# Performance work log

Hardware: AMD Instinct MI355X
Metric: run time of the kernel (lower is better)

The kernel has to match this reference:

```python
import jax, jax.numpy as jnp
import numpy as np

N, E, G, F_IN, H, C = 50000, 800000, 512, 128, 96, 10
BN_EPS = 1e-5


def _bn(x, w, b):
    # torch BatchNorm1d training-mode forward: batch stats, biased variance
    mu = jnp.mean(x, axis=0)
    var = jnp.var(x, axis=0)
    return (x - mu) * jax.lax.rsqrt(var + BN_EPS) * w + b


def setup_inputs() -> dict:
    key = jax.random.key(0)
    ks = iter(jax.random.split(key, 64))

    def rn(shape, s=0.05):
        return jax.random.normal(next(ks), shape, jnp.float32) * s

    inp = {
        "x": jax.random.normal(next(ks), (N, F_IN), jnp.float32),
        "edge_index": jax.random.randint(next(ks), (2, E), 0, N, dtype=jnp.int32),
        "batch": jnp.sort(jax.random.randint(next(ks), (N,), 0, G, dtype=jnp.int32)),
        "bn_feat_w": jnp.ones((F_IN,), jnp.float32),
        "bn_feat_b": jnp.full((F_IN,), 1e-4, jnp.float32),
        "Wf": rn((F_IN, H)), "bf": jnp.zeros((H,), jnp.float32),
        "bn_fc_w": jnp.ones((H,), jnp.float32),
        "bn_fc_b": jnp.full((H,), 1e-4, jnp.float32),
        "Wl": rn((H, H)), "bl": jnp.zeros((H,), jnp.float32),
        "bn_hid_w": jnp.ones((H,), jnp.float32),
        "bn_hid_b": jnp.full((H,), 1e-4, jnp.float32),
        "Wc": rn((H, C)), "bc": jnp.zeros((C,), jnp.float32),
    }
    for i in range(3):
        inp[f"W1_{i}"] = rn((H, H)); inp[f"b1_{i}"] = jnp.zeros((H,), jnp.float32)
        inp[f"bnw_{i}"] = jnp.ones((H,), jnp.float32)
        inp[f"bnb_{i}"] = jnp.full((H,), 1e-4, jnp.float32)
        inp[f"W2_{i}"] = rn((H, H)); inp[f"b2_{i}"] = jnp.zeros((H,), jnp.float32)
    return inp


def reference(x, edge_index, batch, bn_feat_w, bn_feat_b, Wf, bf,
              W1_0, b1_0, bnw_0, bnb_0, W2_0, b2_0,
              W1_1, b1_1, bnw_1, bnb_1, W2_1, b2_1,
              W1_2, b1_2, bnw_2, bnb_2, W2_2, b2_2,
              bn_fc_w, bn_fc_b, Wl, bl, bn_hid_w, bn_hid_b, Wc, bc):
    src, dst = edge_index[0], edge_index[1]
    h = _bn(x, bn_feat_w, bn_feat_b)
    # GCNConv(gfn=True): pure linear feature transform, no propagation
    h = jax.nn.relu(h @ Wf + bf)
    gin_params = [
        (W1_0, b1_0, bnw_0, bnb_0, W2_0, b2_0),
        (W1_1, b1_1, bnw_1, bnb_1, W2_1, b2_1),
        (W1_2, b1_2, bnw_2, bnb_2, W2_2, b2_2),
    ]
    for W1, b1, bw, bb, W2, b2 in gin_params:
        # GIN: (1+eps)*x + sum-aggregate of neighbor features (eps=0)
        agg = jax.ops.segment_sum(h[src], dst, num_segments=N)  # [N, H]
        m = h + agg
        m = jax.nn.relu(_bn(m @ W1 + b1, bw, bb))
        h = jax.nn.relu(m @ W2 + b2)
    # global_add_pool over graphs
    g = jax.ops.segment_sum(h, batch, num_segments=G)  # [G, H]
    g = jax.nn.relu(_bn(g, bn_fc_w, bn_fc_b) @ Wl + bl)
    g = _bn(g, bn_hid_w, bn_hid_b)
    logits = g @ Wc + bc
    return jax.nn.log_softmax(logits, axis=-1)
```

## Files before the change

### kernel.cpp

```cpp
#include <hip/hip_runtime.h>

#define N_NODES 50000
#define N_EDGES 800000
#define N_GRAPHS 512
#define F_IN 128
#define HDIM 96
#define NCLS 10
#define BN_EPS 1e-5f

#define NPB 128
#define NBUCK2 ((N_NODES + NPB - 1) / NPB)
#define NEB 128
#define EPB ((N_EDGES + NEB - 1) / NEB)

typedef unsigned int u32;
typedef unsigned short u16;
typedef __attribute__((ext_vector_type(8))) short bf16x8;
typedef __attribute__((ext_vector_type(4))) float f32x4;

__device__ __forceinline__ u16 f2bf(float f) {
    u32 u = __float_as_uint(f);
    u32 r = (u + 0x7fffu + ((u >> 16) & 1u)) >> 16;
    return (u16)r;
}
__device__ __forceinline__ float bflo(u32 w) { return __uint_as_float(w << 16); }
__device__ __forceinline__ float bfhi(u32 w) { return __uint_as_float(w & 0xffff0000u); }
__device__ __forceinline__ float bf2f(u16 v) { return __uint_as_float((u32)v << 16); }

template<int NC>
__global__ __launch_bounds__(256) void colstats4_kernel(const float* __restrict__ in,
                                                        float* __restrict__ partials,
                                                        int nrows) {
    constexpr int CG  = NC / 4;
    constexpr int RPB = 256 / CG;
    const int cg = threadIdx.x % CG;
    const int rg = threadIdx.x / CG;
    float4 s = make_float4(0.f, 0.f, 0.f, 0.f);
    float4 q = make_float4(0.f, 0.f, 0.f, 0.f);
    for (int r = blockIdx.x * RPB + rg; r < nrows; r += gridDim.x * RPB) {
        float4 v = *(const float4*)&in[(size_t)r * NC + cg * 4];
        s.x += v.x; s.y += v.y; s.z += v.z; s.w += v.w;
        q.x += v.x * v.x; q.y += v.y * v.y; q.z += v.z * v.z; q.w += v.w * v.w;
    }
    __shared__ float ss[RPB][NC], sq[RPB][NC];
    *(float4*)&ss[rg][cg * 4] = s;
    *(float4*)&sq[rg][cg * 4] = q;
    __syncthreads();
    if (threadIdx.x < NC) {
        float a = 0.f, b = 0.f;
        #pragma unroll
        for (int r = 0; r < RPB; r++) { a += ss[r][threadIdx.x]; b += sq[r][threadIdx.x]; }
        partials[(size_t)blockIdx.x * 2 * NC + threadIdx.x]      = a;
        partials[(size_t)blockIdx.x * 2 * NC + NC + threadIdx.x] = b;
    }
}

template<int NCOLS>
__global__ __launch_bounds__(NCOLS * 8) void reduce_finalize_kernel(
        const float* __restrict__ partials, int nslots,
        const float* __restrict__ w,
        const float* __restrict__ b,
        float* __restrict__ ac, float inv_n) {
    const int k   = threadIdx.x % NCOLS;
    const int grp = threadIdx.x / NCOLS;
    const int stride = 2 * NCOLS;
    float s = 0.f, q = 0.f;
    for (int i = grp; i < nslots; i += 8) {
        s += partials[(size_t)i * stride + k];
        q += partials[(size_t)i * stride + NCOLS + k];
    }
    __shared__ float ss[8][NCOLS], sq[8][NCOLS];
    ss[grp][k] = s; sq[grp][k] = q;
    __syncthreads();
    if (grp == 0) {
        float S = ((ss[0][k] + ss[1][k]) + (ss[2][k] + ss[3][k]))
                + ((ss[4][k] + ss[5][k]) + (ss[6][k] + ss[7][k]));
        float Q = ((sq[0][k] + sq[1][k]) + (sq[2][k] + sq[3][k]))
                + ((sq[4][k] + sq[5][k]) + (sq[6][k] + sq[7][k]));
        float mu  = S * inv_n;
        float var = Q * inv_n - mu * mu;
        float a   = w[k] * rsqrtf(var + BN_EPS);
        ac[k]         = a;
        ac[NCOLS + k] = b[k] - mu * a;
    }
}

#define WPF_BLOCKS 48
#define WPH_BLOCKS 36
__global__ __launch_bounds__(256) void wprep_all_kernel(
        const float* __restrict__ Wf, const float* __restrict__ bf, const float* __restrict__ acX,
        const float* __restrict__ W0a, const float* __restrict__ b0a,
        const float* __restrict__ W0b, const float* __restrict__ b0b,
        const float* __restrict__ W1a, const float* __restrict__ b1a,
        const float* __restrict__ W1b, const float* __restrict__ b1b,
        const float* __restrict__ W2a, const float* __restrict__ b2a,
        const float* __restrict__ W2b, const float* __restrict__ b2b,
        u16* __restrict__ wtF, float* __restrict__ bFm,
        u16* __restrict__ wtbase, float* __restrict__ bmbase) {
    const int tid = threadIdx.x;
    int blk = blockIdx.x;
    if (blk < WPF_BLOCKS) {
        int i = blk * 256 + tid;
        if (i < F_IN * 96) {
            int k = i / 96, n = i % 96;
            wtF[n * F_IN + k] = f2bf(Wf[i] * acX[k]);
        }
        if (blk == 0 && tid < 96) {
            float b = bf[tid];
            for (int k = 0; k < F_IN; k++) b += acX[F_IN + k] * Wf[k * 96 + tid];
            bFm[tid] = b;
        }
        return;
    }
    blk -= WPF_BLOCKS;
    const int s  = blk / WPH_BLOCKS;
    const int b2 = blk % WPH_BLOCKS;
    const float* W; const float* bias;
    switch (s) {
        case 0: W = W0a; bias = b0a; break;
        case 1: W = W0b; bias = b0b; break;
        case 2: W = W1a; bias = b1a; break;
        case 3: W = W1b; bias = b1b; break;
        case 4: W = W2a; bias = b2a; break;
        default: W = W2b; bias = b2b; break;
    }
    u16*   wtb  = wtbase + (size_t)s * 96 * HDIM;
    float* bmod = bmbase + (size_t)s * 96;
    int i = b2 * 256 + tid;
    if (i < HDIM * 96) {
        int k = i / 96, n = i % 96;
        wtb[n * HDIM + k] = f2bf(W[i]);
    }
    if (b2 == 0 && tid < 96) bmod[tid] = bias[tid];
}

__global__ __launch_bounds__(1024) void scan1_fused_kernel(
        const int* __restrict__ inA, int nA, int* __restrict__ tmpA, int* __restrict__ partA,
        const int* __restrict__ inB, int nB, int* __restrict__ tmpB, int* __restrict__ partB,
        int nblkA) {
    const int* in; int n; int* tmp; int* partial; int base;
    if ((int)blockIdx.x < nblkA) { in = inA; n = nA; tmp = tmpA; partial = partA; base = blockIdx.x; }
    else                         { in = inB; n = nB; tmp = tmpB; partial = partB; base = blockIdx.x - nblkA; }
    __shared__ int sh[1024];
    const int i = base * 1024 + threadIdx.x;
    const int d = (i < n) ? in[i] : 0;
    sh[threadIdx.x] = d;
    __syncthreads();
    for (int off = 1; off < 1024; off <<= 1) {
        int v = 0;
        if (threadIdx.x >= off) v = sh[threadIdx.x - off];
        __syncthreads();
        sh[threadIdx.x] += v;
        __syncthreads();
    }
    if (i < n) tmp[i] = sh[threadIdx.x] - d;
    if (threadIdx.x == 1023) partial[base] = sh[1023];
}

__global__ __launch_bounds__(1024) void scan3_fused_kernel(
        const int* __restrict__ tmpA, const int* __restrict__ partA,
        const int* __restrict__ degA, int* __restrict__ row_ptr, int nA, int npA,
        const int* __restrict__ tmpB, const int* __restrict__ partB,
        int* __restrict__ ofs, int nB, int npB, int nblkA) {
    const int* tmp; const int* partial; int n, nparts, base; bool isA;
    if ((int)blockIdx.x < nblkA) { tmp = tmpA; partial = partA; n = nA; nparts = npA; base = blockIdx.x; isA = true; }
    else                         { tmp = tmpB; partial = partB; n = nB; nparts = npB; base = blockIdx.x - nblkA; isA = false; }
    __shared__ int offs;
    if (threadIdx.x < 64) {
        int v = (threadIdx.x < base && (int)threadIdx.x < nparts) ? partial[threadIdx.x] : 0;
        for (int o = 32; o > 0; o >>= 1) v += __shfl_down(v, o, 64);
        if (threadIdx.x == 0) offs = v;
    }
    __syncthreads();
    const int i = base * 1024 + threadIdx.x;
    if (i < n) {
        int v = tmp[i] + offs;
        if (isA) {
            row_ptr[i] = v;
            if (i == n - 1) row_ptr[n] = v + degA[i];
        } else {
            ofs[i] = v;
        }
    }
}

__global__ __launch_bounds__(256) void count_kernel(const int* __restrict__ dst,
                                                    int* __restrict__ deg,
                                                    int* __restrict__ cnt) {
    __shared__ int lc[NBUCK2];
    for (int i = threadIdx.x; i < NBUCK2; i += 256) lc[i] = 0;
    __syncthreads();
    const int lo = blockIdx.x * EPB;
    const int hi = min(lo + EPB, N_EDGES);
    for (int e = lo + threadIdx.x; e < hi; e += 256) {
        int d = dst[e];
        atomicAdd(&lc[d / NPB], 1);
        atomicAdd(&deg[d], 1);
    }
    __syncthreads();
    for (int i = threadIdx.x; i < NBUCK2; i += 256)
        cnt[i * NEB + blockIdx.x] = lc[i];
}

__global__ __launch_bounds__(256) void distribute_kernel(const int* __restrict__ src,
                                                         const int* __restrict__ dst,
                                                         const int* __restrict__ ofs,
                                                         u32* __restrict__ ebuf) {
    __shared__ int lofs[NBUCK2];
    for (int i = threadIdx.x; i < NBUCK2; i += 256) lofs[i] = ofs[i * NEB + blockIdx.x];
    __syncthreads();
    const int lo = blockIdx.x * EPB;
    const int hi = min(lo + EPB, N_EDGES);
    for (int e = lo + threadIdx.x; e < hi; e += 256) {
        int d = dst[e];
        int q = atomicAdd(&lofs[d / NPB], 1);
        ebuf[q] = ((u32)src[e] << 7) | (u32)(d & (NPB - 1));
    }
}

__global__ __launch_bounds__(256) void bucket_fill_kernel(const u32* __restrict__ ebuf,
                                                          const int* __restrict__ ofs,
                                                          const int* __restrict__ row_ptr,
                                                          int* __restrict__ csr) {
    __shared__ int cur[NPB];
    const int p    = blockIdx.x;
    const int base = p * NPB;
    const int nn   = min(NPB, N_NODES - base);
    for (int i = threadIdx.x; i < nn; i += 256) cur[i] = row_ptr[base + i];
    __syncthreads();
    const int e0 = ofs[p * NEB];
    const int e1 = (p + 1 < NBUCK2) ? ofs[(p + 1) * NEB] : N_EDGES;
    for (int e = e0 + threadIdx.x; e < e1; e += 256) {
        u32 v = ebuf[e];
        int pos = atomicAdd(&cur[v & (NPB - 1)], 1);
        csr[pos] = (int)(v >> 7);
    }
}

__global__ __launch_bounds__(256) void aggmm_kernel(const u16* __restrict__ hb,
                                                    const int* __restrict__ row_ptr,
                                                    const int* __restrict__ csr,
                                                    const u16* __restrict__ wt,
                                                    const float* __restrict__ bias,
                                                    float* __restrict__ tf,
                                                    float* __restrict__ partials,
                                                    int nrows) {
    constexpr int KP = HDIM + 8;
    constexpr int KB = HDIM / 32;
    __shared__ u16 wlds[96 * KP];
    __shared__ u16 alds[64 * KP];
    __shared__ float sred[2][4][96];
    const int tid = threadIdx.x;

    for (int i = tid; i < 96 * (HDIM / 8); i += 256) {
        int nn = i / (HDIM / 8), c8 = i % (HDIM / 8);
        *(uint4*)&wlds[nn * KP + c8 * 8] = *(const uint4*)&wt[nn * HDIM + c8 * 8];
    }

    const int w    = tid >> 6;
    const int lane = tid & 63;
    const int r16  = lane & 15;
    const int kg   = lane >> 4;
    const int m0   = w * 16;
    float bn[6];
    #pragma unroll
    for (int nt = 0; nt < 6; nt++) bn[nt] = bias[nt * 16 + r16];
    float scol[6] = {0,0,0,0,0,0}, qcol[6] = {0,0,0,0,0,0};

    const int nchunks = (nrows + 63) / 64;
    for (int chunk = blockIdx.x; chunk < nchunks; chunk += gridDim.x) {
        const int row0 = chunk * 64;
        __syncthreads();
        for (int t = tid; t < 64 * 12; t += 256) {
            const int r  = t / 12, sl = t % 12;
            const int node = row0 + r;
            uint4 ov = make_uint4(0u, 0u, 0u, 0u);
            if (node < nrows) {
                const int p0 = row_ptr[node], p1 = row_ptr[node + 1];
                uint4 sv = *(const uint4*)&hb[(size_t)node * 96 + sl * 8];
                double a0 = bflo(sv.x), a1 = bfhi(sv.x), a2 = bflo(sv.y), a3 = bfhi(sv.y);
                double a4 = bflo(sv.z), a5 = bfhi(sv.z), a6 = bflo(sv.w), a7 = bfhi(sv.w);
                int p = p0;
                for (; p + 4 <= p1; p += 4) {
                    int s0 = csr[p], s1 = csr[p + 1], s2 = csr[p + 2], s3 = csr[p + 3];
                    uint4 v0 = *(const uint4*)&hb[(size_t)s0 * 96 + sl * 8];
                    uint4 v1 = *(const uint4*)&hb[(size_t)s1 * 96 + sl * 8];
                    uint4 v2 = *(const uint4*)&hb[(size_t)s2 * 96 + sl * 8];
                    uint4 v3 = *(const uint4*)&hb[(size_t)s3 * 96 + sl * 8];
                    a0 += bflo(v0.x); a0 += bflo(v1.x); a0 += bflo(v2.x); a0 += bflo(v3.x);
                    a1 += bfhi(v0.x); a1 += bfhi(v1.x); a1 += bfhi(v2.x); a1 += bfhi(v3.x);
                    a2 += bflo(v0.y); a2 += bflo(v1.y); a2 += bflo(v2.y); a2 += bflo(v3.y);
                    a3 += bfhi(v0.y); a3 += bfhi(v1.y); a3 += bfhi(v2.y); a3 += bfhi(v3.y);
                    a4 += bflo(v0.z); a4 += bflo(v1.z); a4 += bflo(v2.z); a4 += bflo(v3.z);
                    a5 += bfhi(v0.z); a5 += bfhi(v1.z); a5 += bfhi(v2.z); a5 += bfhi(v3.z);
                    a6 += bflo(v0.w); a6 += bflo(v1.w); a6 += bflo(v2.w); a6 += bflo(v3.w);
                    a7 += bfhi(v0.w); a7 += bfhi(v1.w); a7 += bfhi(v2.w); a7 += bfhi(v3.w);
                }
                for (; p < p1; p++) {
                    int s = csr[p];
                    uint4 v = *(const uint4*)&hb[(size_t)s * 96 + sl * 8];
                    a0 += bflo(v.x); a1 += bfhi(v.x); a2 += bflo(v.y); a3 += bfhi(v.y);
                    a4 += bflo(v.z); a5 += bfhi(v.z); a6 += bflo(v.w); a7 += bfhi(v.w);
                }
                ov.x = (u32)f2bf((float)a0) | ((u32)f2bf((float)a1) << 16);
                ov.y = (u32)f2bf((float)a2) | ((u32)f2bf((float)a3) << 16);
                ov.z = (u32)f2bf((float)a4) | ((u32)f2bf((float)a5) << 16);
                ov.w = (u32)f2bf((float)a6) | ((u32)f2bf((float)a7) << 16);
            }
            *(uint4*)&alds[r * KP + sl * 8] = ov;
        }
        __syncthreads();

        bf16x8 af[KB];
        #pragma unroll
        for (int kb = 0; kb < KB; kb++)
            af[kb] = *(const bf16x8*)&alds[(m0 + r16) * KP + kb * 32 + kg * 8];

        f32x4 acc[6];
        #pragma unroll
        for (int nt = 0; nt < 6; nt++) acc[nt] = (f32x4){bn[nt], bn[nt], bn[nt], bn[nt]};
        #pragma unroll
        for (int kb = 0; kb < KB; kb++) {
            #pragma unroll
            for (int nt = 0; nt < 6; nt++) {
                bf16x8 bfr = *(const bf16x8*)&wlds[(nt * 16 + r16) * KP + kb * 32 + kg * 8];
                acc[nt] = __builtin_amdgcn_mfma_f32_16x16x32_bf16(af[kb], bfr, acc[nt], 0, 0, 0);
            }
        }

        const int gr0  = row0 + m0 + kg * 4;
        const bool full = (gr0 + 3 < nrows);
        #pragma unroll
        for (int nt = 0; nt < 6; nt++) {
            const int n = nt * 16 + r16;
            #pragma unroll
            for (int rr = 0; rr < 4; rr++) {
                const int gr = gr0 + rr;
                if (full || gr < nrows) {
                    float v = acc[nt][rr];
                    tf[(size_t)gr * 96 + n] = v;
                    scol[nt] += v; qcol[nt] += v * v;
                }
            }
        }
    }

    #pragma unroll
    for (int nt = 0; nt < 6; nt++) {
        scol[nt] += __shfl_xor(scol[nt], 16);
        scol[nt] += __shfl_xor(scol[nt], 32);
        qcol[nt] += __shfl_xor(qcol[nt], 16);
        qcol[nt] += __shfl_xor(qcol[nt], 32);
    }
    __syncthreads();
    if (kg == 0) {
        #pragma unroll
        for (int nt = 0; nt < 6; nt++) {
            sred[0][w][nt * 16 + r16] = scol[nt];
            sred[1][w][nt * 16 + r16] = qcol[nt];
        }
    }
    __syncthreads();
    if (tid < 96) {
        float a = (sred[0][0][tid] + sred[0][1][tid]) + (sred[0][2][tid] + sred[0][3][tid]);
        float b = (sred[1][0][tid] + sred[1][1][tid]) + (sred[1][2][tid] + sred[1][3][tid]);
        partials[(size_t)blockIdx.x * 192 + tid]      = a;
        partials[(size_t)blockIdx.x * 192 + 96 + tid] = b;
    }
}

template<int KDIM, bool IN_F32, bool IN_AFF_RELU, bool OUT_RELU, bool STATS, bool OUT_BF16>
__global__ __launch_bounds__(256) void mmx_kernel(const void* __restrict__ in_,
                                                  const u16* __restrict__ wt,
                                                  const float* __restrict__ bias,
                                                  const float* __restrict__ ac,
                                                  void* __restrict__ out_,
                                                  float* __restrict__ partials,
                                                  int nrows) {
    constexpr int KP = KDIM + 8;
    constexpr int KB = KDIM / 32;
    __shared__ u16 wlds[96 * KP];
    __shared__ u16 alds[64 * KP];
    __shared__ float sred[2][4][96];
    const int tid = threadIdx.x;

    for (int i = tid; i < 96 * (KDIM / 8); i += 256) {
        int nn = i / (KDIM / 8), c8 = i % (KDIM / 8);
        *(uint4*)&wlds[nn * KP + c8 * 8] = *(const uint4*)&wt[nn * KDIM + c8 * 8];
    }

    const int w    = tid >> 6;
    const int lane = tid & 63;
    const int r16  = lane & 15;
    const int kg   = lane >> 4;
    const int m0   = w * 16;
    float bn[6];
    #pragma unroll
    for (int nt = 0; nt < 6; nt++) bn[nt] = bias[nt * 16 + r16];
    float scol[6] = {0,0,0,0,0,0}, qcol[6] = {0,0,0,0,0,0};

    const int nchunks = (nrows + 63) / 64;
    for (int chunk = blockIdx.x; chunk < nchunks; chunk += gridDim.x) {
        const int row0 = chunk * 64;
        __syncthreads();
        if constexpr (IN_F32) {
            const float* inf = (const float*)in_;
            for (int i = tid; i < 64 * (KDIM / 4); i += 256) {
                int r = i / (KDIM / 4), c4 = i % (KDIM / 4);
                int gr = row0 + r;
                float4 v = (gr < nrows) ? *(const float4*)&inf[(size_t)gr * KDIM + c4 * 4]
                                        : make_float4(0.f, 0.f, 0.f, 0.f);
                if constexpr (IN_AFF_RELU) {
                    float4 a = *(const float4*)&ac[c4 * 4];
                    float4 c = *(const float4*)&ac[KDIM + c4 * 4];
                    v.x = fmaxf(v.x * a.x + c.x, 0.f);
                    v.y = fmaxf(v.y * a.y + c.y, 0.f);
                    v.z = fmaxf(v.z * a.z + c.z, 0.f);
                    v.w = fmaxf(v.w * a.w + c.w, 0.f);
                }
                ushort4 o; o.x = f2bf(v.x); o.y = f2bf(v.y); o.z = f2bf(v.z); o.w = f2bf(v.w);
                *(ushort4*)&alds[r * KP + c4 * 4] = o;
            }
        } else {
            const u16* inb = (const u16*)in_;
            for (int i = tid; i < 64 * (KDIM / 8); i += 256) {
                int r = i / (KDIM / 8), c8 = i % (KDIM / 8);
                int gr = row0 + r;
                uint4 v = (gr < nrows) ? *(const uint4*)&inb[(size_t)gr * KDIM + c8 * 8]
                                       : make_uint4(0u, 0u, 0u, 0u);
                *(uint4*)&alds[r * KP + c8 * 8] = v;
            }
        }
        __syncthreads();

        bf16x8 af[KB];
        #pragma unroll
        for (int kb = 0; kb < KB; kb++)
            af[kb] = *(const bf16x8*)&alds[(m0 + r16) * KP + kb * 32 + kg * 8];

        f32x4 acc[6];
        #pragma unroll
        for (int nt = 0; nt < 6; nt++) acc[nt] = (f32x4){bn[nt], bn[nt], bn[nt], bn[nt]};
        #pragma unroll
        for (int kb = 0; kb < KB; kb++) {
            #pragma unroll
            for (int nt = 0; nt < 6; nt++) {
                bf16x8 bfr = *(const bf16x8*)&wlds[(nt * 16 + r16) * KP + kb * 32 + kg * 8];
                acc[nt] = __builtin_amdgcn_mfma_f32_16x16x32_bf16(af[kb], bfr, acc[nt], 0, 0, 0);
            }
        }

        const int gr0  = row0 + m0 + kg * 4;
        const bool full = (gr0 + 3 < nrows);
        #pragma unroll
        for (int nt = 0; nt < 6; nt++) {
            float v[4] = {acc[nt][0], acc[nt][1], acc[nt][2], acc[nt][3]};
            if constexpr (OUT_RELU) {
                #pragma unroll
                for (int rr = 0; rr < 4; rr++) v[rr] = fmaxf(v[rr], 0.f);
            }
            const int n = nt * 16 + r16;
            #pragma unroll
            for (int rr = 0; rr < 4; rr++) {
                const int gr = gr0 + rr;
                if (full || gr < nrows) {
                    if constexpr (OUT_BF16) ((u16*)out_)[(size_t)gr * 96 + n] = f2bf(v[rr]);
                    else                    ((float*)out_)[(size_t)gr * 96 + n] = v[rr];
                    if constexpr (STATS) { scol[nt] += v[rr]; qcol[nt] += v[rr] * v[rr]; }
                }
            }
        }
    }

    if constexpr (STATS) {
        #pragma unroll
        for (int nt = 0; nt < 6; nt++) {
            scol[nt] += __shfl_xor(scol[nt], 16);
            scol[nt] += __shfl_xor(scol[nt], 32);
            qcol[nt] += __shfl_xor(qcol[nt], 16);
            qcol[nt] += __shfl_xor(qcol[nt], 32);
        }
        __syncthreads();
        if (kg == 0) {
            #pragma unroll
            for (int nt = 0; nt < 6; nt++) {
                sred[0][w][nt * 16 + r16] = scol[nt];
                sred[1][w][nt * 16 + r16] = qcol[nt];
            }
        }
        __syncthreads();
        if (tid < 96) {
            float a = (sred[0][0][tid] + sred[0][1][tid]) + (sred[0][2][tid] + sred[0][3][tid]);
            float b = (sred[1][0][tid] + sred[1][1][tid]) + (sred[1][2][tid] + sred[1][3][tid]);
            partials[(size_t)blockIdx.x * 192 + tid]      = a;
            partials[(size_t)blockIdx.x * 192 + 96 + tid] = b;
        }
    }
}

__device__ __forceinline__ int lower_bound_dev(const int* __restrict__ a, int n, int v) {
    int lo = 0, hi = n;
    while (lo < hi) { int m = (lo + hi) >> 1; if (a[m] < v) lo = m + 1; else hi = m; }
    return lo;
}
__global__ __launch_bounds__(96) void pool_stats_kernel(const u16* __restrict__ hb,
                                                        const int* __restrict__ batch,
                                                        float* __restrict__ g,
                                                        float* __restrict__ partials) {
    const int gi = blockIdx.x;
    __shared__ int sh_lo, sh_hi;
    if (threadIdx.x == 0) sh_lo = lower_bound_dev(batch, N_NODES, gi);
    if (threadIdx.x == 1) sh_hi = lower_bound_dev(batch, N_NODES, gi + 1);
    __syncthreads();
    const int lo = sh_lo, hi = sh_hi;
    const int j = threadIdx.x;
    float s0 = 0.f, s1 = 0.f, s2 = 0.f, s3 = 0.f;
    int r = lo;
    for (; r + 4 <= hi; r += 4) {
        s0 += bf2f(hb[(size_t)r       * 96 + j]);
        s1 += bf2f(hb[(size_t)(r + 1) * 96 + j]);
        s2 += bf2f(hb[(size_t)(r + 2) * 96 + j]);
        s3 += bf2f(hb[(size_t)(r + 3) * 96 + j]);
    }
    for (; r < hi; r++) s0 += bf2f(hb[(size_t)r * 96 + j]);
    float val = (s0 + s1) + (s2 + s3);
    g[(size_t)gi * 96 + j] = val;
    partials[(size_t)gi * 192 + j]      = val;
    partials[(size_t)gi * 192 + 96 + j] = val * val;
}

template<int KDIM, bool IN_AFF, bool IN_RELU, bool OUT_RELU, bool STATS>
__global__ __launch_bounds__(192) void mm_kernel(const float* __restrict__ in,
                                                 const float* __restrict__ W,
                                                 const float* __restrict__ bias,
                                                 const float* __restrict__ ac,
                                                 float* __restrict__ out,
                                                 float* __restrict__ partials, int nrows) {
    constexpr int KG = KDIM / 4;
    __shared__ float ws[KDIM][96];
    __shared__ float xs[32][KDIM];
    const int tid = threadIdx.x;
    const int cg  = tid % 24;
    const int rg  = tid / 24;
    for (int i = tid; i < KDIM * 24; i += 192) {
        int k = i / 24, c4 = i % 24;
        *(float4*)&ws[k][c4 * 4] = *(const float4*)&W[(size_t)k * 96 + c4 * 4];
    }
    const float4 bj = *(const float4*)&bias[cg * 4];
    float s0=0,s1=0,s2=0,s3=0, q0=0,q1=0,q2=0,q3=0;
    const int nchunks = (nrows + 31) / 32;
    for (int chunk = blockIdx.x; chunk < nchunks; chunk += gridDim.x) {
        const int row0 = chunk * 32;
        __syncthreads();
        for (int i = tid; i < 32 * KG; i += 192) {
            int r = i / KG, g = i % KG;
            int gr = row0 + r;
            float4 v = make_float4(0.f, 0.f, 0.f, 0.f);
            if (gr < nrows) v = *(const float4*)&in[(size_t)gr * KDIM + g * 4];
            if constexpr (IN_AFF) {
                float4 a = *(const float4*)&ac[g * 4];
                float4 c = *(const float4*)&ac[KDIM + g * 4];
                v.x = v.x * a.x + c.x; v.y = v.y * a.y + c.y;
                v.z = v.z * a.z + c.z; v.w = v.w * a.w + c.w;
            }
            if constexpr (IN_RELU) {
                v.x = fmaxf(v.x, 0.f); v.y = fmaxf(v.y, 0.f);
                v.z = fmaxf(v.z, 0.f); v.w = fmaxf(v.w, 0.f);
            }
            *(float4*)&xs[r][4 * (g ^ (r & 7))] = v;
        }
        __syncthreads();
        float acc[4][4];
        #pragma unroll
        for (int m = 0; m < 4; m++) {
            acc[m][0] = bj.x; acc[m][1] = bj.y; acc[m][2] = bj.z; acc[m][3] = bj.w;
        }
        #pragma unroll 4
        for (int g = 0; g < KG; g++) {
            const int xi = 4 * (g ^ rg);
            float4 xv0 = *(const float4*)&xs[rg     ][xi];
            float4 xv1 = *(const float4*)&xs[rg +  8][xi];
            float4 xv2 = *(const float4*)&xs[rg + 16][xi];
            float4 xv3 = *(const float4*)&xs[rg + 24][xi];
            #pragma unroll
            for (int i = 0; i < 4; i++) {
                float4 wv = *(const float4*)&ws[g * 4 + i][cg * 4];
                float x0 = (i==0)?xv0.x:(i==1)?xv0.y:(i==2)?xv0.z:xv0.w;
                float x1 = (i==0)?xv1.x:(i==1)?xv1.y:(i==2)?xv1.z:xv1.w;
                float x2 = (i==0)?xv2.x:(i==1)?xv2.y:(i==2)?xv2.z:xv2.w;
                float x3 = (i==0)?xv3.x:(i==1)?xv3.y:(i==2)?xv3.z:xv3.w;
                acc[0][0] = fmaf(x0, wv.x, acc[0][0]); acc[0][1] = fmaf(x0, wv.y, acc[0][1]);
                acc[0][2] = fmaf(x0, wv.z, acc[0][2]); acc[0][3] = fmaf(x0, wv.w, acc[0][3]);
                acc[1][0] = fmaf(x1, wv.x, acc[1][0]); acc[1][1] = fmaf(x1, wv.y, acc[1][1]);
                acc[1][2] = fmaf(x1, wv.z, acc[1][2]); acc[1][3] = fmaf(x1, wv.w, acc[1][3]);
                acc[2][0] = fmaf(x2, wv.x, acc[2][0]); acc[2][1] = fmaf(x2, wv.y, acc[2][1]);
                acc[2][2] = fmaf(x2, wv.z, acc[2][2]); acc[2][3] = fmaf(x2, wv.w, acc[2][3]);
                acc[3][0] = fmaf(x3, wv.x, acc[3][0]); acc[3][1] = fmaf(x3, wv.y, acc[3][1]);
                acc[3][2] = fmaf(x3, wv.z, acc[3][2]); acc[3][3] = fmaf(x3, wv.w, acc[3][3]);
            }
        }
        #pragma unroll
        for (int m = 0; m < 4; m++) {
            const int gr = row0 + rg + 8 * m;
            if (gr < nrows) {
                float4 o = make_float4(acc[m][0], acc[m][1], acc[m][2], acc[m][3]);
                if constexpr (OUT_RELU) {
                    o.x = fmaxf(o.x, 0.f); o.y = fmaxf(o.y, 0.f);
                    o.z = fmaxf(o.z, 0.f); o.w = fmaxf(o.w, 0.f);
                }
                *(float4*)&out[(size_t)gr * 96 + cg * 4] = o;
                if constexpr (STATS) {
                    s0 += o.x; q0 += o.x * o.x; s1 += o.y; q1 += o.y * o.y;
                    s2 += o.z; q2 += o.z * o.z; s3 += o.w; q3 += o.w * o.w;
                }
            }
        }
    }
    if constexpr (STATS) {
        __syncthreads();
        float* rs = &xs[0][0];
        float* rq = rs + 8 * 96;
        rs[rg * 96 + cg * 4 + 0] = s0; rs[rg * 96 + cg * 4 + 1] = s1;
        rs[rg * 96 + cg * 4 + 2] = s2; rs[rg * 96 + cg * 4 + 3] = s3;
        rq[rg * 96 + cg * 4 + 0] = q0; rq[rg * 96 + cg * 4 + 1] = q1;
        rq[rg * 96 + cg * 4 + 2] = q2; rq[rg * 96 + cg * 4 + 3] = q3;
        __syncthreads();
        if (tid < 96) {
            float a = 0.f, b = 0.f;
            #pragma unroll
            for (int r = 0; r < 8; r++) { a += rs[r * 96 + tid]; b += rq[r * 96 + tid]; }
            partials[(size_t)blockIdx.x * 192 + tid]      = a;
            partials[(size_t)blockIdx.x * 192 + 96 + tid] = b;
        }
    }
}

__global__ void head_kernel(const float* __restrict__ g1, const float* __restrict__ ac,
                            const float* __restrict__ Wc, const float* __restrict__ bc,
                            float* __restrict__ out, int ngraphs) {
    int gi = blockIdx.x * blockDim.x + threadIdx.x;
    if (gi >= ngraphs) return;
    float v[NCLS];
    #pragma unroll
    for (int c = 0; c < NCLS; c++) v[c] = bc[c];
    for (int k = 0; k < HDIM; k++) {
        float x = g1[(size_t)gi * HDIM + k] * ac[k] + ac[HDIM + k];
        #pragma unroll
        for (int c = 0; c < NCLS; c++) v[c] = fmaf(x, Wc[k * NCLS + c], v[c]);
    }
    float mx = v[0];
    #pragma unroll
    for (int c = 1; c < NCLS; c++) mx = fmaxf(mx, v[c]);
    float sum = 0.f;
    #pragma unroll
    for (int c = 0; c < NCLS; c++) sum += expf(v[c] - mx);
    float lse = mx + logf(sum);
    #pragma unroll
    for (int c = 0; c < NCLS; c++) out[(size_t)gi * NCLS + c] = v[c] - lse;
}

extern "C" void kernel_launch(void* const* d_in, const int* in_sizes, int n_in,
                              void* d_out, int out_size, void* d_ws, size_t ws_size,
                              hipStream_t stream) {
    const float* x         = (const float*)d_in[0];
    const int*   ei        = (const int*)  d_in[1];
    const int*   batch     = (const int*)  d_in[2];
    const float* bn_feat_w = (const float*)d_in[3];
    const float* bn_feat_b = (const float*)d_in[4];
    const float* Wf        = (const float*)d_in[5];
    const float* bfv       = (const float*)d_in[6];
    const float* bn_fc_w   = (const float*)d_in[7];
    const float* bn_fc_b   = (const float*)d_in[8];
    const float* Wl        = (const float*)d_in[9];
    const float* bl        = (const float*)d_in[10];
    const float* bn_hid_w  = (const float*)d_in[11];
    const float* bn_hid_b  = (const float*)d_in[12];
    const float* Wc        = (const float*)d_in[13];
    const float* bc        = (const float*)d_in[14];
    float* out = (float*)d_out;

    char* p = (char*)d_ws;
    auto alloc = [&](size_t bytes) { char* q = p; p += (bytes + 255) & ~(size_t)255; return q; };

    int*   deg    = (int*)  alloc((size_t)N_NODES * 4);

    float* pstatX = (float*)alloc((size_t)256 * 2 * F_IN * 4);
    float* pstatT = (float*)alloc((size_t)1024 * 192 * 4);
    float* pstatG = (float*)alloc((size_t)N_GRAPHS * 192 * 4);
    float* pstatG1= (float*)alloc((size_t)16 * 192 * 4);

    u16*   hb     = (u16*)  alloc((size_t)N_NODES * HDIM * 2);
    float* tf     = (float*)alloc((size_t)N_NODES * HDIM * 4);
    float* g      = (float*)alloc((size_t)N_GRAPHS * HDIM * 4);
    float* g1     = (float*)alloc((size_t)N_GRAPHS * HDIM * 4);
    float* acX    = (float*)alloc(2 * F_IN * 4);
    float* acT    = (float*)alloc(2 * HDIM * 4);
    float* acG    = (float*)alloc(2 * HDIM * 4);
    float* acHid  = (float*)alloc(2 * HDIM * 4);
    u16*   wtF    = (u16*)  alloc(96 * F_IN * 2);
    float* bFmod  = (float*)alloc(96 * 4);
    u16*   wtH    = (u16*)  alloc((size_t)6 * 96 * HDIM * 2);
    float* bmH    = (float*)alloc((size_t)6 * 96 * 4);
    int* row_ptr  = (int*)alloc((size_t)(N_NODES + 1) * 4);
    int* csr      = (int*)alloc((size_t)N_EDGES * 4);
    int* stmp     = (int*)alloc((size_t)N_NODES * 4);
    int* spart    = (int*)alloc(64 * 4);
    int* cnt      = (int*)alloc((size_t)NBUCK2 * NEB * 4);
    int* ofs      = (int*)alloc((size_t)NBUCK2 * NEB * 4);
    int* stmp2    = (int*)alloc((size_t)NBUCK2 * NEB * 4);
    int* spart2   = (int*)alloc(64 * 4);
    u32* ebuf     = (u32*)alloc((size_t)N_EDGES * 4);

    const int* srcp = ei;
    const int* dstp = ei + N_EDGES;

    const int nch64  = (N_NODES + 63) / 64;
    const int gridF  = (nch64 < 768) ? nch64 : 768;
    const int grid96 = (nch64 < 1024) ? nch64 : 1024;
    const int gridG  = (N_GRAPHS + 31) / 32;
    const int nscan  = (N_NODES + 1023) / 1024;
    const int ncb    = NBUCK2 * NEB;
    const int nscan2 = (ncb + 1023) / 1024;

    hipMemsetAsync(deg, 0, (size_t)N_NODES * 4, stream);

    colstats4_kernel<F_IN><<<256, 256, 0, stream>>>(x, pstatX, N_NODES);
    reduce_finalize_kernel<F_IN><<<1, F_IN * 8, 0, stream>>>(pstatX, 256, bn_feat_w, bn_feat_b, acX, 1.0f / N_NODES);
    wprep_all_kernel<<<WPF_BLOCKS + 6 * WPH_BLOCKS, 256, 0, stream>>>(
        Wf, bfv, acX,
        (const float*)d_in[15], (const float*)d_in[16],
        (const float*)d_in[19], (const float*)d_in[20],
        (const float*)d_in[21], (const float*)d_in[22],
        (const float*)d_in[25], (const float*)d_in[26],
        (const float*)d_in[27], (const float*)d_in[28],
        (const float*)d_in[31], (const float*)d_in[32],
        wtF, bFmod, wtH, bmH);
    mmx_kernel<F_IN, true, false, true, false, true><<<gridF, 256, 0, stream>>>(x, wtF, bFmod, nullptr, hb, nullptr, N_NODES);

    count_kernel<<<NEB, 256, 0, stream>>>(dstp, deg, cnt);
    scan1_fused_kernel<<<nscan + nscan2, 1024, 0, stream>>>(deg, N_NODES, stmp, spart,
                                                            cnt, ncb, stmp2, spart2, nscan);
    scan3_fused_kernel<<<nscan + nscan2, 1024, 0, stream>>>(stmp, spart, deg, row_ptr, N_NODES, nscan,
                                                            stmp2, spart2, ofs, ncb, nscan2, nscan);
    distribute_kernel<<<NEB, 256, 0, stream>>>(srcp, dstp, ofs, ebuf);
    bucket_fill_kernel<<<NBUCK2, 256, 0, stream>>>(ebuf, ofs, row_ptr, csr);

    for (int l = 0; l < 3; l++) {
        const float* bw = (const float*)d_in[17 + 6 * l];
        const float* bb = (const float*)d_in[18 + 6 * l];
        u16*   wt1 = wtH + (size_t)(2 * l)     * 96 * HDIM;
        u16*   wt2 = wtH + (size_t)(2 * l + 1) * 96 * HDIM;
        float* b1m = bmH + (size_t)(2 * l)     * 96;
        float* b2m = bmH + (size_t)(2 * l + 1) * 96;
        aggmm_kernel<<<grid96, 256, 0, stream>>>(hb, row_ptr, csr, wt1, b1m, tf, pstatT, N_NODES);
        reduce_finalize_kernel<HDIM><<<1, HDIM * 8, 0, stream>>>(pstatT, grid96, bw, bb, acT, 1.0f / N_NODES);
        mmx_kernel<HDIM, true, true, true, false, true><<<grid96, 256, 0, stream>>>(tf, wt2, b2m, acT, hb, nullptr, N_NODES);
    }

    pool_stats_kernel<<<N_GRAPHS, 96, 0, stream>>>(hb, batch, g, pstatG);
    reduce_finalize_kernel<HDIM><<<1, HDIM * 8, 0, stream>>>(pstatG, N_GRAPHS, bn_fc_w, bn_fc_b, acG, 1.0f / N_GRAPHS);
    mm_kernel<HDIM, true, false, true, true><<<gridG, 192, 0, stream>>>(g, Wl, bl, acG, g1, pstatG1, N_GRAPHS);
    reduce_finalize_kernel<HDIM><<<1, HDIM * 8, 0, stream>>>(pstatG1, gridG, bn_hid_w, bn_hid_b, acHid, 1.0f / N_GRAPHS);

    head_kernel<<<2, 256, 0, stream>>>(g1, acHid, Wc, bc, out, N_GRAPHS);
}
```

Before: 392.3 us.

## Derive row_ptr inside bucket fill via local per-bucket scan, drop global degree pass

The global per-node degree histogram (with 800k global atomics), its memset, and the node-level scan are removed. Each bucket block now counts its own nodes' edges in shared memory, scans them locally, writes row_ptr from the bucket's edge offset, and then scatters into the CSR. This trades global atomics and scan traffic for an extra pass over each bucket's edge buffer in the fill kernel.

Result: faster. 359.0 us (-8.5%).

```diff
diff --git a/kernel.cpp b/kernel.cpp
--- a/kernel.cpp
+++ b/kernel.cpp
@@ -134,15 +134,25 @@
     if (b2 == 0 && tid < 96) bmod[tid] = bias[tid];
 }
 
-__global__ __launch_bounds__(1024) void scan1_fused_kernel(
-        const int* __restrict__ inA, int nA, int* __restrict__ tmpA, int* __restrict__ partA,
-        const int* __restrict__ inB, int nB, int* __restrict__ tmpB, int* __restrict__ partB,
-        int nblkA) {
-    const int* in; int n; int* tmp; int* partial; int base;
-    if ((int)blockIdx.x < nblkA) { in = inA; n = nA; tmp = tmpA; partial = partA; base = blockIdx.x; }
-    else                         { in = inB; n = nB; tmp = tmpB; partial = partB; base = blockIdx.x - nblkA; }
+__global__ __launch_bounds__(256) void count_kernel(const int* __restrict__ dst,
+                                                    int* __restrict__ cnt) {
+    __shared__ int lc[NBUCK2];
+    for (int i = threadIdx.x; i < NBUCK2; i += 256) lc[i] = 0;
+    __syncthreads();
+    const int lo = blockIdx.x * EPB;
+    const int hi = min(lo + EPB, N_EDGES);
+    for (int e = lo + threadIdx.x; e < hi; e += 256)
+        atomicAdd(&lc[dst[e] / NPB], 1);
+    __syncthreads();
+    for (int i = threadIdx.x; i < NBUCK2; i += 256)
+        cnt[i * NEB + blockIdx.x] = lc[i];
+}
+
+__global__ __launch_bounds__(1024) void scan1_kernel(const int* __restrict__ in,
+                                                     int* __restrict__ tmp,
+                                                     int* __restrict__ partial, int n) {
     __shared__ int sh[1024];
-    const int i = base * 1024 + threadIdx.x;
+    const int i = blockIdx.x * 1024 + threadIdx.x;
     const int d = (i < n) ? in[i] : 0;
     sh[threadIdx.x] = d;
     __syncthreads();
@@ -154,52 +164,22 @@
         __syncthreads();
     }
     if (i < n) tmp[i] = sh[threadIdx.x] - d;
-    if (threadIdx.x == 1023) partial[base] = sh[1023];
-}
-
-__global__ __launch_bounds__(1024) void scan3_fused_kernel(
-        const int* __restrict__ tmpA, const int* __restrict__ partA,
-        const int* __restrict__ degA, int* __restrict__ row_ptr, int nA, int npA,
-        const int* __restrict__ tmpB, const int* __restrict__ partB,
-        int* __restrict__ ofs, int nB, int npB, int nblkA) {
-    const int* tmp; const int* partial; int n, nparts, base; bool isA;
-    if ((int)blockIdx.x < nblkA) { tmp = tmpA; partial = partA; n = nA; nparts = npA; base = blockIdx.x; isA = true; }
-    else                         { tmp = tmpB; partial = partB; n = nB; nparts = npB; base = blockIdx.x - nblkA; isA = false; }
+    if (threadIdx.x == 1023) partial[blockIdx.x] = sh[1023];
+}
+
+__global__ __launch_bounds__(1024) void scan3_kernel(const int* __restrict__ tmp,
+                                                     const int* __restrict__ partial,
+                                                     int* __restrict__ out,
+                                                     int n, int nparts) {
     __shared__ int offs;
     if (threadIdx.x < 64) {
-        int v = (threadIdx.x < base && (int)threadIdx.x < nparts) ? partial[threadIdx.x] : 0;
+        int v = (threadIdx.x < blockIdx.x && (int)threadIdx.x < nparts) ? partial[threadIdx.x] : 0;
         for (int o = 32; o > 0; o >>= 1) v += __shfl_down(v, o, 64);
         if (threadIdx.x == 0) offs = v;
     }
     __syncthreads();
-    const int i = base * 1024 + threadIdx.x;
-    if (i < n) {
-        int v = tmp[i] + offs;
-        if (isA) {
-            row_ptr[i] = v;
-            if (i == n - 1) row_ptr[n] = v + degA[i];
-        } else {
-            ofs[i] = v;
-        }
-    }
-}
-
-__global__ __launch_bounds__(256) void count_kernel(const int* __restrict__ dst,
-                                                    int* __restrict__ deg,
-                                                    int* __restrict__ cnt) {
-    __shared__ int lc[NBUCK2];
-    for (int i = threadIdx.x; i < NBUCK2; i += 256) lc[i] = 0;
-    __syncthreads();
-    const int lo = blockIdx.x * EPB;
-    const int hi = min(lo + EPB, N_EDGES);
-    for (int e = lo + threadIdx.x; e < hi; e += 256) {
-        int d = dst[e];
-        atomicAdd(&lc[d / NPB], 1);
-        atomicAdd(&deg[d], 1);
-    }
-    __syncthreads();
-    for (int i = threadIdx.x; i < NBUCK2; i += 256)
-        cnt[i * NEB + blockIdx.x] = lc[i];
+    const int i = blockIdx.x * 1024 + threadIdx.x;
+    if (i < n) out[i] = tmp[i] + offs;
 }
 
 __global__ __launch_bounds__(256) void distribute_kernel(const int* __restrict__ src,
@@ -218,21 +198,41 @@
     }
 }
 
-__global__ __launch_bounds__(256) void bucket_fill_kernel(const u32* __restrict__ ebuf,
-                                                          const int* __restrict__ ofs,
-                                                          const int* __restrict__ row_ptr,
-                                                          int* __restrict__ csr) {
-    __shared__ int cur[NPB];
+__global__ __launch_bounds__(256) void bucket_fill2_kernel(const u32* __restrict__ ebuf,
+                                                           const int* __restrict__ ofs,
+                                                           int* __restrict__ row_ptr,
+                                                           int* __restrict__ csr) {
+    __shared__ int lcnt[NPB], lpos[NPB];
     const int p    = blockIdx.x;
     const int base = p * NPB;
     const int nn   = min(NPB, N_NODES - base);
-    for (int i = threadIdx.x; i < nn; i += 256) cur[i] = row_ptr[base + i];
-    __syncthreads();
+    const int tid  = threadIdx.x;
     const int e0 = ofs[p * NEB];
     const int e1 = (p + 1 < NBUCK2) ? ofs[(p + 1) * NEB] : N_EDGES;
-    for (int e = e0 + threadIdx.x; e < e1; e += 256) {
+    for (int i = tid; i < NPB; i += 256) lcnt[i] = 0;
+    __syncthreads();
+    for (int e = e0 + tid; e < e1; e += 256)
+        atomicAdd(&lcnt[ebuf[e] & (NPB - 1)], 1);
+    __syncthreads();
+    if (tid < NPB) lpos[tid] = lcnt[tid];
+    __syncthreads();
+    for (int off = 1; off < NPB; off <<= 1) {
+        int v = 0;
+        if (tid < NPB && tid >= off) v = lpos[tid - off];
+        __syncthreads();
+        if (tid < NPB) lpos[tid] += v;
+        __syncthreads();
+    }
+    if (tid < NPB) {
+        int excl = lpos[tid] - lcnt[tid];
+        lpos[tid] = e0 + excl;
+        if (tid < nn) row_ptr[base + tid] = e0 + excl;
+    }
+    if (p == NBUCK2 - 1 && tid == 0) row_ptr[N_NODES] = N_EDGES;
+    __syncthreads();
+    for (int e = e0 + tid; e < e1; e += 256) {
         u32 v = ebuf[e];
-        int pos = atomicAdd(&cur[v & (NPB - 1)], 1);
+        int pos = atomicAdd(&lpos[v & (NPB - 1)], 1);
         csr[pos] = (int)(v >> 7);
     }
 }
@@ -682,8 +682,6 @@
     char* p = (char*)d_ws;
     auto alloc = [&](size_t bytes) { char* q = p; p += (bytes + 255) & ~(size_t)255; return q; };
 
-    int*   deg    = (int*)  alloc((size_t)N_NODES * 4);
-
     float* pstatX = (float*)alloc((size_t)256 * 2 * F_IN * 4);
     float* pstatT = (float*)alloc((size_t)1024 * 192 * 4);
     float* pstatG = (float*)alloc((size_t)N_GRAPHS * 192 * 4);
@@ -703,8 +701,6 @@
     float* bmH    = (float*)alloc((size_t)6 * 96 * 4);
     int* row_ptr  = (int*)alloc((size_t)(N_NODES + 1) * 4);
     int* csr      = (int*)alloc((size_t)N_EDGES * 4);
-    int* stmp     = (int*)alloc((size_t)N_NODES * 4);
-    int* spart    = (int*)alloc(64 * 4);
     int* cnt      = (int*)alloc((size_t)NBUCK2 * NEB * 4);
     int* ofs      = (int*)alloc((size_t)NBUCK2 * NEB * 4);
     int* stmp2    = (int*)alloc((size_t)NBUCK2 * NEB * 4);
@@ -718,11 +714,8 @@
     const int gridF  = (nch64 < 768) ? nch64 : 768;
     const int grid96 = (nch64 < 1024) ? nch64 : 1024;
     const int gridG  = (N_GRAPHS + 31) / 32;
-    const int nscan  = (N_NODES + 1023) / 1024;
     const int ncb    = NBUCK2 * NEB;
     const int nscan2 = (ncb + 1023) / 1024;
-
-    hipMemsetAsync(deg, 0, (size_t)N_NODES * 4, stream);
 
     colstats4_kernel<F_IN><<<256, 256, 0, stream>>>(x, pstatX, N_NODES);
     reduce_finalize_kernel<F_IN><<<1, F_IN * 8, 0, stream>>>(pstatX, 256, bn_feat_w, bn_feat_b, acX, 1.0f / N_NODES);
@@ -737,13 +730,11 @@
         wtF, bFmod, wtH, bmH);
     mmx_kernel<F_IN, true, false, true, false, true><<<gridF, 256, 0, stream>>>(x, wtF, bFmod, nullptr, hb, nullptr, N_NODES);
 
-    count_kernel<<<NEB, 256, 0, stream>>>(dstp, deg, cnt);
-    scan1_fused_kernel<<<nscan + nscan2, 1024, 0, stream>>>(deg, N_NODES, stmp, spart,
-                                                            cnt, ncb, stmp2, spart2, nscan);
-    scan3_fused_kernel<<<nscan + nscan2, 1024, 0, stream>>>(stmp, spart, deg, row_ptr, N_NODES, nscan,
-                                                            stmp2, spart2, ofs, ncb, nscan2, nscan);
+    count_kernel<<<NEB, 256, 0, stream>>>(dstp, cnt);
+    scan1_kernel<<<nscan2, 1024, 0, stream>>>(cnt, stmp2, spart2, ncb);
+    scan3_kernel<<<nscan2, 1024, 0, stream>>>(stmp2, spart2, ofs, ncb, nscan2);
     distribute_kernel<<<NEB, 256, 0, stream>>>(srcp, dstp, ofs, ebuf);
-    bucket_fill_kernel<<<NBUCK2, 256, 0, stream>>>(ebuf, ofs, row_ptr, csr);
+    bucket_fill2_kernel<<<NBUCK2, 256, 0, stream>>>(ebuf, ofs, row_ptr, csr);
 
     for (int l = 0; l < 3; l++) {
         const float* bw = (const float*)d_in[17 + 6 * l];
```
